# Performance work log

Hardware: AMD Instinct MI355X
Metric: run time of the kernel (lower is better)

## Reference

```python
import jax, jax.numpy as jnp
import numpy as np
from itertools import product

B, C, HH, WW, DD, N = 2, 32, 96, 96, 96, 30000


def setup_inputs() -> dict:
    key = jax.random.key(0)
    k1, k2, k3 = jax.random.split(key, 3)
    voxel_features = jax.random.normal(k1, (B, C, HH, WW, DD), dtype=jnp.float32)
    # vertices in normalized [-1, 1] grid_sample coordinates (x, y, z)
    vertices = jax.random.uniform(k2, (B, N, 3), dtype=jnp.float32, minval=-1.0, maxval=1.0)
    fan_in = C * 27
    conv_w = jax.random.normal(k3, (C, C, 1, 27), dtype=jnp.float32) * np.sqrt(2.0 / fan_in)
    conv_b = jnp.zeros((C,), dtype=jnp.float32)
    return {
        "voxel_features": voxel_features,
        "vertices": vertices,
        "conv_w": conv_w,
        "conv_b": conv_b,
        "img_H": HH,
        "img_W": WW,
        "img_D": DD,
    }


def _trilinear_sample(voxel_features, grid):
    """grid_sample(mode='bilinear', padding_mode='border', align_corners=True).
    voxel_features: (B,C,H,W,D); grid: (B,N,K,3) with (x,y,z) in [-1,1],
    x -> D axis, y -> W axis, z -> H axis. Returns (B,C,N,K)."""
    b, c, h, w, d = voxel_features.shape
    x, y, z = grid[..., 0], grid[..., 1], grid[..., 2]
    ix = jnp.clip((x + 1.0) * 0.5 * (d - 1), 0.0, d - 1)
    iy = jnp.clip((y + 1.0) * 0.5 * (w - 1), 0.0, w - 1)
    iz = jnp.clip((z + 1.0) * 0.5 * (h - 1), 0.0, h - 1)
    x0 = jnp.floor(ix).astype(jnp.int32); x1 = jnp.minimum(x0 + 1, d - 1)
    y0 = jnp.floor(iy).astype(jnp.int32); y1 = jnp.minimum(y0 + 1, w - 1)
    z0 = jnp.floor(iz).astype(jnp.int32); z1 = jnp.minimum(z0 + 1, h - 1)
    fx = ix - x0; fy = iy - y0; fz = iz - z0
    vf = voxel_features.reshape(b, c, h * w * d)
    n, k = grid.shape[1], grid.shape[2]

    def gather(zi, yi, xi):
        lin = (zi * w + yi) * d + xi  # (B,N,K)
        g = jnp.take_along_axis(vf, lin.reshape(b, 1, n * k), axis=2)
        return g.reshape(b, c, n, k)

    def wgt(wz, wy, wx):
        return (wz * wy * wx)[:, None]  # (B,1,N,K)

    out = (
        gather(z0, y0, x0) * wgt(1 - fz, 1 - fy, 1 - fx)
        + gather(z0, y0, x1) * wgt(1 - fz, 1 - fy, fx)
        + gather(z0, y1, x0) * wgt(1 - fz, fy, 1 - fx)
        + gather(z0, y1, x1) * wgt(1 - fz, fy, fx)
        + gather(z1, y0, x0) * wgt(fz, 1 - fy, 1 - fx)
        + gather(z1, y0, x1) * wgt(fz, 1 - fy, fx)
        + gather(z1, y1, x0) * wgt(fz, fy, 1 - fx)
        + gather(z1, y1, x1) * wgt(fz, fy, fx)
    )
    return out


def reference(voxel_features, vertices, conv_w, conv_b, img_H, img_W, img_D):
    # 27 neighbor offsets in normalized coords, scaled per (x,y,z) component
    offs = jnp.asarray(list(product((-1, 0, 1), repeat=3)), dtype=jnp.float32)  # (27,3)
    scale = jnp.array(
        [2.0 / (img_D - 1), 2.0 / (img_W - 1), 2.0 / (img_H - 1)], dtype=jnp.float32
    )
    shift = offs * scale  # (27,3)
    grid = vertices[:, :, None, :] + shift[None, None]  # (B,N,27,3)
    feats = _trilinear_sample(voxel_features, grid)  # (B,C,N,27)
    # Conv2d(C,C,(1,27)): weighted reduction over (C_in, 27) -> (B,N,C_out)
    out = jnp.einsum("bink,oik->bno", feats, conv_w[:, :, 0, :]) + conv_b
    return out
```

## Files before the change

kernel.cpp:

```cpp
#include <hip/hip_runtime.h>
#include <stdint.h>

#define HWD 884736ull
#define NV 30000
#define AST 1032

typedef __attribute__((ext_vector_type(8))) __bf16 bf16x8;
typedef __attribute__((ext_vector_type(4))) float f32x4;
typedef __attribute__((ext_vector_type(2))) unsigned int uint2v;
typedef __attribute__((ext_vector_type(4))) unsigned int uint4v;

__device__ __forceinline__ unsigned short f2bf(float f) {
    union { float f; unsigned int u; } v; v.f = f;
    unsigned int u = v.u;
    return (unsigned short)((u + 0x7FFFu + ((u >> 16) & 1u)) >> 16);
}

__device__ __forceinline__ float bf_lo(unsigned int u) {
    union { unsigned int u; float f; } v; v.u = u << 16; return v.f;
}
__device__ __forceinline__ float bf_hi(unsigned int u) {
    union { unsigned int u; float f; } v; v.u = u & 0xffff0000u; return v.f;
}

__device__ __forceinline__ void axis_setup(float coord, float sc, int& wstart, float w[3][4]) {
    int i0[3], i1[3];
    float fr[3];
#pragma unroll
    for (int a = 0; a < 3; ++a) {
        float g = coord + (float)(a - 1) * sc;
        float ix = (g + 1.0f) * 0.5f * 95.0f;
        ix = fminf(fmaxf(ix, 0.0f), 95.0f);
        float fl = floorf(ix);
        int x0 = (int)fl;
        i0[a] = x0;
        i1[a] = min(x0 + 1, 95);
        fr[a] = ix - fl;
    }
    int ws = min(max(i0[1] - 1, 0), 92);
    wstart = ws;
#pragma unroll
    for (int a = 0; a < 3; ++a) {
        int d0 = min(max(i0[a] - ws, 0), 3);
        int d1 = min(max(i1[a] - ws, 0), 3);
        float f1 = fr[a], f0 = 1.0f - f1;
#pragma unroll
        for (int j = 0; j < 4; ++j)
            w[a][j] = (d0 == j ? f0 : 0.0f) + (d1 == j ? f1 : 0.0f);
    }
}

__global__ __launch_bounds__(256) void prep_kernel(const float* __restrict__ cw,
                                                   unsigned short* __restrict__ Wp) {
    int gid = blockIdx.x * 256 + threadIdx.x;
    int j = gid & 7;
    int l = (gid >> 3) & 63;
    int t = (gid >> 9) & 1;
    int s = gid >> 10;
    int kk = ((l >> 4) & 3) * 8 + j;
    int o = t * 16 + (l & 15);
    float v = 0.0f;
    if (kk < 27) v = cw[(size_t)o * 864 + s * 27 + kk];
    Wp[gid] = f2bf(v);
}

__global__ __launch_bounds__(256) void transpose_kernel(const float* __restrict__ vox,
                                                        uint2v* __restrict__ voxQ) {
    int blk = blockIdx.x;
    int tid = threadIdx.x;
    int b = blk / 9216;
    int zy = blk % 9216;
    const float* src = vox + (size_t)b * 32 * HWD + (size_t)zy * 96;
    uint2v* dst = voxQ + (size_t)blk * 768;
#pragma unroll
    for (int i = 0; i < 3; ++i) {
        int idx = i * 256 + tid;
        int c = idx & 31;
        int q = idx >> 5;
        f32x4 v = *(const f32x4*)(src + (size_t)c * HWD + q * 4);
        unsigned int u0 = (unsigned int)f2bf(v[0]) | ((unsigned int)f2bf(v[1]) << 16);
        unsigned int u1 = (unsigned int)f2bf(v[2]) | ((unsigned int)f2bf(v[3]) << 16);
        uint2v p = {u0, u1};
        dst[q * 32 + c] = p;
    }
}

__global__ __launch_bounds__(512) void fused_kernel(const uint2v* __restrict__ voxQ,
                                                    const float* __restrict__ verts,
                                                    const unsigned short* __restrict__ Wp,
                                                    const float* __restrict__ bias,
                                                    float* __restrict__ out) {
    __shared__ __align__(16) unsigned short At[16 * AST];
    int tid = threadIdx.x;
    int vl = tid >> 5;
    int c = tid & 31;
    int vg = (int)blockIdx.x * 16 + vl;

    const float* vp = verts + (size_t)vg * 3;
    float vx = vp[0], vy = vp[1], vz = vp[2];
    const float sc = 2.0f / 95.0f;
    int wsx, wsy, wsz;
    float wx[3][4], wy[3][4], wz[3][4];
    axis_setup(vx, sc, wsx, wx);
    axis_setup(vy, sc, wsy, wy);
    axis_setup(vz, sc, wsz, wz);

    int o = wsx & 3;
    bool s1 = (o & 1) != 0, s2 = (o & 2) != 0;
    float wx7[3][7];
#pragma unroll
    for (int a = 0; a < 3; ++a) {
        float t0 = s1 ? 0.0f : wx[a][0];
        float t1 = s1 ? wx[a][0] : wx[a][1];
        float t2 = s1 ? wx[a][1] : wx[a][2];
        float t3 = s1 ? wx[a][2] : wx[a][3];
        float t4 = s1 ? wx[a][3] : 0.0f;
        wx7[a][0] = s2 ? 0.0f : t0;
        wx7[a][1] = s2 ? 0.0f : t1;
        wx7[a][2] = s2 ? t0 : t2;
        wx7[a][3] = s2 ? t1 : t3;
        wx7[a][4] = s2 ? t2 : t4;
        wx7[a][5] = s2 ? t3 : 0.0f;
        wx7[a][6] = s2 ? t4 : 0.0f;
    }
    int q0 = wsx >> 2;
    int q1 = min(q0 + 1, 23);

    int bb = (vg >= NV) ? 1 : 0;
    const uint2v* Qb = voxQ + (size_t)bb * 9216 * 768 + c;

    float f[27];
#pragma unroll
    for (int k = 0; k < 27; ++k) f[k] = 0.0f;

#pragma unroll
    for (int tz = 0; tz < 4; ++tz) {
        float ry[9];
#pragma unroll
        for (int i = 0; i < 9; ++i) ry[i] = 0.0f;
#pragma unroll
        for (int ty = 0; ty < 4; ++ty) {
            size_t r = ((size_t)(wsz + tz) * 96 + (size_t)(wsy + ty)) * 24;
            uint2v A = Qb[(r + q0) * 32];
            uint2v Bq = Qb[(r + q1) * 32];
            float b0 = bf_lo(A[0]), b1 = bf_hi(A[0]), b2 = bf_lo(A[1]), b3 = bf_hi(A[1]);
            float b4 = bf_lo(Bq[0]), b5 = bf_hi(Bq[0]), b6 = bf_lo(Bq[1]);
#pragma unroll
            for (int a = 0; a < 3; ++a) {
                float rxt = b0 * wx7[a][0] + b1 * wx7[a][1] + b2 * wx7[a][2] +
                            b3 * wx7[a][3] + b4 * wx7[a][4] + b5 * wx7[a][5] +
                            b6 * wx7[a][6];
#pragma unroll
                for (int b = 0; b < 3; ++b)
                    ry[3 * b + a] = fmaf(rxt, wy[b][ty], ry[3 * b + a]);
            }
        }
#pragma unroll
        for (int g = 0; g < 3; ++g)
#pragma unroll
            for (int b = 0; b < 3; ++b)
#pragma unroll
                for (int a = 0; a < 3; ++a)
                    f[9 * a + 3 * b + g] = fmaf(ry[3 * b + a], wz[g][tz], f[9 * a + 3 * b + g]);
    }

    unsigned short* rowp = &At[vl * AST];
#pragma unroll
    for (int j = 0; j < 4; ++j) {
        const int kb = j * 8;
        unsigned int pw[4];
#pragma unroll
        for (int t2 = 0; t2 < 4; ++t2) {
            int k0 = kb + 2 * t2, k1 = k0 + 1;
            float lo = (k0 < 27) ? f[k0] : 0.0f;
            float hi = (k1 < 27) ? f[k1] : 0.0f;
            pw[t2] = (unsigned int)f2bf(lo) | ((unsigned int)f2bf(hi) << 16);
        }
        uint4v s = {pw[0], pw[1], pw[2], pw[3]};
        int p = c * 4 + ((j + c) & 3);
        *(uint4v*)(rowp + p * 8) = s;
    }

    __syncthreads();

    int wv = tid >> 6;
    if (wv < 2) {
        int lane = tid & 63;
        int mrow = lane & 15, quad = lane >> 4;
        const bf16x8* wp = (const bf16x8*)Wp;
        f32x4 acc = {0.f, 0.f, 0.f, 0.f};
#pragma unroll 8
        for (int s = 0; s < 32; ++s) {
            int p = s * 4 + ((quad + s) & 3);
            bf16x8 a = *(const bf16x8*)&At[mrow * AST + p * 8];
            bf16x8 b = wp[(s * 2 + wv) * 64 + lane];
            acc = __builtin_amdgcn_mfma_f32_16x16x32_bf16(a, b, acc, 0, 0, 0);
        }
        float bs = bias[wv * 16 + mrow];
#pragma unroll
        for (int r = 0; r < 4; ++r) {
            int v = (int)blockIdx.x * 16 + quad * 4 + r;
            out[(size_t)v * 32 + wv * 16 + mrow] = acc[r] + bs;
        }
    }
}

extern "C" void kernel_launch(void* const* d_in, const int* in_sizes, int n_in,
                              void* d_out, int out_size, void* d_ws, size_t ws_size,
                              hipStream_t stream) {
    const float* vox = (const float*)d_in[0];
    const float* verts = (const float*)d_in[1];
    const float* cw = (const float*)d_in[2];
    const float* cb = (const float*)d_in[3];
    float* out = (float*)d_out;

    unsigned short* Wp = (unsigned short*)d_ws;
    uint2v* voxQ = (uint2v*)((char*)d_ws + 65536);

    hipLaunchKernelGGL(prep_kernel, dim3(128), dim3(256), 0, stream, cw, Wp);
    hipLaunchKernelGGL(transpose_kernel, dim3(18432), dim3(256), 0, stream, vox, voxQ);
    hipLaunchKernelGGL(fused_kernel, dim3(3750), dim3(512), 0, stream,
                       voxQ, verts, Wp, cb, out);
}
```

Baseline: 457.1 us.

## Bucket-sort vertices by batch and z-slice to improve gather locality

Adds a single-block histogram/scan kernel and a scatter kernel that build a permutation of vertices grouped by batch and z voxel index. The fused sampling kernel then processes vertices in that order and writes outputs through the permutation, so that nearby blocks touch similar z-slabs of the bf16 voxel tensor and reuse cache. This costs two extra launches, one of them serialized on a single block iterating 60000 vertices, plus scattered output writes.

```diff
diff --git a/kernel.cpp b/kernel.cpp
--- a/kernel.cpp
+++ b/kernel.cpp
@@ -3,7 +3,9 @@
 
 #define HWD 884736ull
 #define NV 30000
+#define NVT 60000
 #define AST 1032
+#define NBKT 192
 
 typedef __attribute__((ext_vector_type(8))) __bf16 bf16x8;
 typedef __attribute__((ext_vector_type(4))) float f32x4;
@@ -21,6 +23,14 @@
 }
 __device__ __forceinline__ float bf_hi(unsigned int u) {
     union { unsigned int u; float f; } v; v.u = u & 0xffff0000u; return v.f;
+}
+
+__device__ __forceinline__ int bucket_key(const float* __restrict__ verts, int v) {
+    float z = verts[(size_t)v * 3 + 2];
+    float iz = fminf(fmaxf((z + 1.0f) * 0.5f * 95.0f, 0.0f), 95.0f);
+    int zv = min((int)iz, 95);
+    int b = (v >= NV) ? 1 : 0;
+    return b * 96 + zv;
 }
 
 __device__ __forceinline__ void axis_setup(float coord, float sc, int& wstart, float w[3][4]) {
@@ -85,18 +95,49 @@
     }
 }
 
+__global__ __launch_bounds__(256) void count_kernel(const float* __restrict__ verts,
+                                                    int* __restrict__ cursors) {
+    __shared__ int hist[NBKT];
+    __shared__ int scan[NBKT];
+    int tid = threadIdx.x;
+    for (int i = tid; i < NBKT; i += 256) hist[i] = 0;
+    __syncthreads();
+    for (int v = tid; v < NVT; v += 256)
+        atomicAdd(&hist[bucket_key(verts, v)], 1);
+    __syncthreads();
+    if (tid == 0) {
+        int acc = 0;
+        for (int i = 0; i < NBKT; ++i) { scan[i] = acc; acc += hist[i]; }
+    }
+    __syncthreads();
+    for (int i = tid; i < NBKT; i += 256) cursors[i] = scan[i];
+}
+
+__global__ __launch_bounds__(256) void scatter_kernel(const float* __restrict__ verts,
+                                                      int* __restrict__ cursors,
+                                                      int* __restrict__ perm) {
+    int v = blockIdx.x * 256 + threadIdx.x;
+    if (v >= NVT) return;
+    int pos = atomicAdd(&cursors[bucket_key(verts, v)], 1);
+    perm[pos] = v;
+}
+
 __global__ __launch_bounds__(512) void fused_kernel(const uint2v* __restrict__ voxQ,
                                                     const float* __restrict__ verts,
                                                     const unsigned short* __restrict__ Wp,
                                                     const float* __restrict__ bias,
+                                                    const int* __restrict__ perm,
                                                     float* __restrict__ out) {
     __shared__ __align__(16) unsigned short At[16 * AST];
+    __shared__ int vids[16];
     int tid = threadIdx.x;
     int vl = tid >> 5;
     int c = tid & 31;
-    int vg = (int)blockIdx.x * 16 + vl;
-
-    const float* vp = verts + (size_t)vg * 3;
+    if (tid < 16) vids[tid] = perm[(int)blockIdx.x * 16 + tid];
+    __syncthreads();
+    int vid = vids[vl];
+
+    const float* vp = verts + (size_t)vid * 3;
     float vx = vp[0], vy = vp[1], vz = vp[2];
     const float sc = 2.0f / 95.0f;
     int wsx, wsy, wsz;
@@ -126,7 +167,7 @@
     int q0 = wsx >> 2;
     int q1 = min(q0 + 1, 23);
 
-    int bb = (vg >= NV) ? 1 : 0;
+    int bb = (vid >= NV) ? 1 : 0;
     const uint2v* Qb = voxQ + (size_t)bb * 9216 * 768 + c;
 
     float f[27];
@@ -199,8 +240,8 @@
         float bs = bias[wv * 16 + mrow];
 #pragma unroll
         for (int r = 0; r < 4; ++r) {
-            int v = (int)blockIdx.x * 16 + quad * 4 + r;
-            out[(size_t)v * 32 + wv * 16 + mrow] = acc[r] + bs;
+            int vrow = vids[quad * 4 + r];
+            out[(size_t)vrow * 32 + wv * 16 + mrow] = acc[r] + bs;
         }
     }
 }
@@ -214,11 +255,17 @@
     const float* cb = (const float*)d_in[3];
     float* out = (float*)d_out;
 
-    unsigned short* Wp = (unsigned short*)d_ws;
-    uint2v* voxQ = (uint2v*)((char*)d_ws + 65536);
+    char* wsp = (char*)d_ws;
+    unsigned short* Wp = (unsigned short*)wsp;
+    int* cursors = (int*)(wsp + 65536);
+    int* perm = (int*)(wsp + 65536 + 1024);
+    uint2v* voxQ = (uint2v*)(wsp + 65536 + 1024 + 245760);
 
     hipLaunchKernelGGL(prep_kernel, dim3(128), dim3(256), 0, stream, cw, Wp);
+    hipLaunchKernelGGL(count_kernel, dim3(1), dim3(256), 0, stream, verts, cursors);
+    hipLaunchKernelGGL(scatter_kernel, dim3((NVT + 255) / 256), dim3(256), 0, stream,
+                       verts, cursors, perm);
     hipLaunchKernelGGL(transpose_kernel, dim3(18432), dim3(256), 0, stream, vox, voxQ);
     hipLaunchKernelGGL(fused_kernel, dim3(3750), dim3(512), 0, stream,
-                       voxQ, verts, Wp, cb, out);
-}
+                       voxQ, verts, Wp, cb, perm, out);
+}
```

Result: slower. 602.7 us (+31.8%).

## Use bf16 dot2 and packed FMAs with double-buffered z-slab loads in fused sampler

Applied to the files above, without the earlier changes.

Rewrites the inner trilinear accumulation of the fused kernel. The x-axis weights are packed to bf16 pairs so the voxel pairs can go through v_dot2 bf16 instructions, and the y/z accumulations use packed float2 FMAs. The next z-slab's voxel loads are prefetched into a double buffer while the current slab is computed, and launch bounds now request 4 blocks per CU. The aims are fewer ALU instructions and more hidden memory latency, at the cost of rounding the x-weights to bf16 and higher register pressure.

```diff
diff --git a/kernel.cpp b/kernel.cpp
--- a/kernel.cpp
+++ b/kernel.cpp
@@ -6,7 +6,9 @@
 #define AST 1032
 
 typedef __attribute__((ext_vector_type(8))) __bf16 bf16x8;
+typedef __attribute__((ext_vector_type(2))) __bf16 bf16x2;
 typedef __attribute__((ext_vector_type(4))) float f32x4;
+typedef __attribute__((ext_vector_type(2))) float f32x2;
 typedef __attribute__((ext_vector_type(2))) unsigned int uint2v;
 typedef __attribute__((ext_vector_type(4))) unsigned int uint4v;
 
@@ -21,6 +23,15 @@
 }
 __device__ __forceinline__ float bf_hi(unsigned int u) {
     union { unsigned int u; float f; } v; v.u = u & 0xffff0000u; return v.f;
+}
+
+__device__ __forceinline__ float dot2bf(unsigned int u, unsigned int w, float acc) {
+#if __has_builtin(__builtin_amdgcn_fdot2_f32_bf16)
+    return __builtin_amdgcn_fdot2_f32_bf16(__builtin_bit_cast(bf16x2, u),
+                                           __builtin_bit_cast(bf16x2, w), acc, false);
+#else
+    return fmaf(bf_hi(u), bf_hi(w), fmaf(bf_lo(u), bf_lo(w), acc));
+#endif
 }
 
 __device__ __forceinline__ void axis_setup(float coord, float sc, int& wstart, float w[3][4]) {
@@ -85,11 +96,11 @@
     }
 }
 
-__global__ __launch_bounds__(512) void fused_kernel(const uint2v* __restrict__ voxQ,
-                                                    const float* __restrict__ verts,
-                                                    const unsigned short* __restrict__ Wp,
-                                                    const float* __restrict__ bias,
-                                                    float* __restrict__ out) {
+__global__ __launch_bounds__(512, 4) void fused_kernel(const uint2v* __restrict__ voxQ,
+                                                       const float* __restrict__ verts,
+                                                       const unsigned short* __restrict__ Wp,
+                                                       const float* __restrict__ bias,
+                                                       float* __restrict__ out) {
     __shared__ __align__(16) unsigned short At[16 * AST];
     int tid = threadIdx.x;
     int vl = tid >> 5;
@@ -105,64 +116,102 @@
     axis_setup(vy, sc, wsy, wy);
     axis_setup(vz, sc, wsz, wz);
 
-    int o = wsx & 3;
-    bool s1 = (o & 1) != 0, s2 = (o & 2) != 0;
-    float wx7[3][7];
-#pragma unroll
-    for (int a = 0; a < 3; ++a) {
-        float t0 = s1 ? 0.0f : wx[a][0];
-        float t1 = s1 ? wx[a][0] : wx[a][1];
-        float t2 = s1 ? wx[a][1] : wx[a][2];
-        float t3 = s1 ? wx[a][2] : wx[a][3];
-        float t4 = s1 ? wx[a][3] : 0.0f;
-        wx7[a][0] = s2 ? 0.0f : t0;
-        wx7[a][1] = s2 ? 0.0f : t1;
-        wx7[a][2] = s2 ? t0 : t2;
-        wx7[a][3] = s2 ? t1 : t3;
-        wx7[a][4] = s2 ? t2 : t4;
-        wx7[a][5] = s2 ? t3 : 0.0f;
-        wx7[a][6] = s2 ? t4 : 0.0f;
-    }
+    unsigned int wxp[3][4];
+    {
+        int o = wsx & 3;
+        bool s1 = (o & 1) != 0, s2 = (o & 2) != 0;
+#pragma unroll
+        for (int a = 0; a < 3; ++a) {
+            unsigned int w01 = (unsigned int)f2bf(wx[a][0]) | ((unsigned int)f2bf(wx[a][1]) << 16);
+            unsigned int w23 = (unsigned int)f2bf(wx[a][2]) | ((unsigned int)f2bf(wx[a][3]) << 16);
+            unsigned int a0 = s1 ? (w01 << 16) : w01;
+            unsigned int a1 = s1 ? ((w01 >> 16) | (w23 << 16)) : w23;
+            unsigned int a2 = s1 ? (w23 >> 16) : 0u;
+            wxp[a][0] = s2 ? 0u : a0;
+            wxp[a][1] = s2 ? a0 : a1;
+            wxp[a][2] = s2 ? a1 : a2;
+            wxp[a][3] = s2 ? a2 : 0u;
+        }
+    }
+    f32x2 wyp[4], wzp[4];
+    float wy2[4], wz2[4];
+#pragma unroll
+    for (int t = 0; t < 4; ++t) {
+        wyp[t] = (f32x2){wy[0][t], wy[1][t]}; wy2[t] = wy[2][t];
+        wzp[t] = (f32x2){wz[0][t], wz[1][t]}; wz2[t] = wz[2][t];
+    }
+
     int q0 = wsx >> 2;
-    int q1 = min(q0 + 1, 23);
-
+    int qd = (q0 < 23) ? 256 : 0;
     int bb = (vg >= NV) ? 1 : 0;
-    const uint2v* Qb = voxQ + (size_t)bb * 9216 * 768 + c;
-
-    float f[27];
-#pragma unroll
-    for (int k = 0; k < 27; ++k) f[k] = 0.0f;
+    const char* pb = (const char*)voxQ + (size_t)bb * 56623104ull +
+                     (size_t)wsz * 589824 + (size_t)wsy * 6144 + (size_t)q0 * 256 + c * 8;
+
+    uint2v bufA[2][4], bufB[2][4];
+#pragma unroll
+    for (int ty = 0; ty < 4; ++ty) {
+        const char* pr = pb + ty * 6144;
+        bufA[0][ty] = *(const uint2v*)pr;
+        bufB[0][ty] = *(const uint2v*)(pr + qd);
+    }
+
+    f32x2 fp[9];
+    float fs[9];
+#pragma unroll
+    for (int i = 0; i < 9; ++i) { fp[i] = (f32x2){0.f, 0.f}; fs[i] = 0.f; }
 
 #pragma unroll
     for (int tz = 0; tz < 4; ++tz) {
-        float ry[9];
-#pragma unroll
-        for (int i = 0; i < 9; ++i) ry[i] = 0.0f;
+        const int cur = tz & 1;
+        if (tz < 3) {
+            const char* pn = pb + (size_t)(tz + 1) * 589824;
+            const int nxt = cur ^ 1;
+#pragma unroll
+            for (int ty = 0; ty < 4; ++ty) {
+                const char* pr = pn + ty * 6144;
+                bufA[nxt][ty] = *(const uint2v*)pr;
+                bufB[nxt][ty] = *(const uint2v*)(pr + qd);
+            }
+        }
+        f32x2 ryp[3];
+        float rys[3];
+#pragma unroll
+        for (int a = 0; a < 3; ++a) { ryp[a] = (f32x2){0.f, 0.f}; rys[a] = 0.f; }
 #pragma unroll
         for (int ty = 0; ty < 4; ++ty) {
-            size_t r = ((size_t)(wsz + tz) * 96 + (size_t)(wsy + ty)) * 24;
-            uint2v A = Qb[(r + q0) * 32];
-            uint2v Bq = Qb[(r + q1) * 32];
-            float b0 = bf_lo(A[0]), b1 = bf_hi(A[0]), b2 = bf_lo(A[1]), b3 = bf_hi(A[1]);
-            float b4 = bf_lo(Bq[0]), b5 = bf_hi(Bq[0]), b6 = bf_lo(Bq[1]);
+            unsigned int A0 = bufA[cur][ty][0], A1 = bufA[cur][ty][1];
+            unsigned int B0 = bufB[cur][ty][0], B1 = bufB[cur][ty][1];
 #pragma unroll
             for (int a = 0; a < 3; ++a) {
-                float rxt = b0 * wx7[a][0] + b1 * wx7[a][1] + b2 * wx7[a][2] +
-                            b3 * wx7[a][3] + b4 * wx7[a][4] + b5 * wx7[a][5] +
-                            b6 * wx7[a][6];
-#pragma unroll
-                for (int b = 0; b < 3; ++b)
-                    ry[3 * b + a] = fmaf(rxt, wy[b][ty], ry[3 * b + a]);
+                float r = dot2bf(B1, wxp[a][3], 0.0f);
+                r = dot2bf(B0, wxp[a][2], r);
+                r = dot2bf(A1, wxp[a][1], r);
+                r = dot2bf(A0, wxp[a][0], r);
+                f32x2 rr = {r, r};
+                ryp[a] = rr * wyp[ty] + ryp[a];
+                rys[a] = fmaf(r, wy2[ty], rys[a]);
             }
         }
 #pragma unroll
-        for (int g = 0; g < 3; ++g)
-#pragma unroll
-            for (int b = 0; b < 3; ++b)
-#pragma unroll
-                for (int a = 0; a < 3; ++a)
-                    f[9 * a + 3 * b + g] = fmaf(ry[3 * b + a], wz[g][tz], f[9 * a + 3 * b + g]);
-    }
+        for (int a = 0; a < 3; ++a)
+#pragma unroll
+            for (int b = 0; b < 3; ++b) {
+                float rv = (b < 2) ? ryp[a][b] : rys[a];
+                f32x2 rr = {rv, rv};
+                fp[3 * a + b] = rr * wzp[tz] + fp[3 * a + b];
+                fs[3 * a + b] = fmaf(rv, wz2[tz], fs[3 * a + b]);
+            }
+    }
+
+    float ff[27];
+#pragma unroll
+    for (int a = 0; a < 3; ++a)
+#pragma unroll
+        for (int b = 0; b < 3; ++b) {
+            ff[9 * a + 3 * b + 0] = fp[3 * a + b][0];
+            ff[9 * a + 3 * b + 1] = fp[3 * a + b][1];
+            ff[9 * a + 3 * b + 2] = fs[3 * a + b];
+        }
 
     unsigned short* rowp = &At[vl * AST];
 #pragma unroll
@@ -172,8 +221,8 @@
 #pragma unroll
         for (int t2 = 0; t2 < 4; ++t2) {
             int k0 = kb + 2 * t2, k1 = k0 + 1;
-            float lo = (k0 < 27) ? f[k0] : 0.0f;
-            float hi = (k1 < 27) ? f[k1] : 0.0f;
+            float lo = (k0 < 27) ? ff[k0] : 0.0f;
+            float hi = (k1 < 27) ? ff[k1] : 0.0f;
             pw[t2] = (unsigned int)f2bf(lo) | ((unsigned int)f2bf(hi) << 16);
         }
         uint4v s = {pw[0], pw[1], pw[2], pw[3]};
```

After: 420.4 us. 8.0% less time.
